# Kernel optimization log

Hardware: AMD Instinct MI355X
Metric: run time of the kernel (lower is better)

Reference implementation:

```python
import jax, jax.numpy as jnp
import numpy as np

B, S, D, H = 2, 2048, 1024, 16
DK = D // H

def setup_inputs() -> dict:
    key = jax.random.key(0)
    ks = jax.random.split(key, 9)
    scale = 1.0 / np.sqrt(D)
    return {
        "x": jax.random.normal(ks[0], (B, S, D), dtype=jnp.float32),
        "Wq": jax.random.uniform(ks[1], (D, D), jnp.float32, -scale, scale),
        "bq": jax.random.uniform(ks[2], (D,), jnp.float32, -scale, scale),
        "Wk": jax.random.uniform(ks[3], (D, D), jnp.float32, -scale, scale),
        "bk": jax.random.uniform(ks[4], (D,), jnp.float32, -scale, scale),
        "Wv": jax.random.uniform(ks[5], (D, D), jnp.float32, -scale, scale),
        "bv": jax.random.uniform(ks[6], (D,), jnp.float32, -scale, scale),
        "Wo": jax.random.uniform(ks[7], (D, D), jnp.float32, -scale, scale),
        "bo": jax.random.uniform(ks[8], (D,), jnp.float32, -scale, scale),
    }

def reference(x, Wq, bq, Wk, bk, Wv, bv, Wo, bo):
    # QKV projections (torch Linear: x @ W.T + b)
    q = x @ Wq.T + bq
    k = x @ Wk.T + bk
    v = x @ Wv.T + bv
    # [B, H, S, DK]
    q = q.reshape(B, S, H, DK).transpose(0, 2, 1, 3)
    k = k.reshape(B, S, H, DK).transpose(0, 2, 1, 3)
    v = v.reshape(B, S, H, DK).transpose(0, 2, 1, 3)
    scores = jnp.einsum('bhqd,bhkd->bhqk', q, k) / jnp.sqrt(jnp.float32(DK))
    p = jax.nn.softmax(scores, axis=-1)  # dropout is identity in eval mode
    o = jnp.einsum('bhqk,bhkd->bhqd', p, v)
    o = o.transpose(0, 2, 1, 3).reshape(B, S, D)
    return o @ Wo.T + bo
```

## Files before the change

### kernel.cpp

```cpp
#include <hip/hip_runtime.h>


typedef __attribute__((ext_vector_type(8))) short short8;
typedef __attribute__((ext_vector_type(4))) float f32x4;
typedef __attribute__((ext_vector_type(8))) unsigned short u16x8;

__device__ __forceinline__ unsigned short f2bf(float f) {
    unsigned int u = __builtin_bit_cast(unsigned int, f);
    u += 0x7FFFu + ((u >> 16) & 1u);
    return (unsigned short)(u >> 16);
}

__device__ __forceinline__ float exp2_fast(float x) {
    return __builtin_amdgcn_exp2f(x);
}

__device__ __forceinline__ void gload16(const void* gsrc, void* ldst) {
    __builtin_amdgcn_global_load_lds(
        (const __attribute__((address_space(1))) unsigned int*)gsrc,
        (__attribute__((address_space(3))) unsigned int*)ldst, 16, 0, 0);
}

__global__ void cast_all(const float* __restrict__ x,
                         const float* __restrict__ wq, const float* __restrict__ wk,
                         const float* __restrict__ wv, const float* __restrict__ wo,
                         unsigned short* __restrict__ xb,
                         unsigned short* __restrict__ wqb, unsigned short* __restrict__ wkb,
                         unsigned short* __restrict__ wvb, unsigned short* __restrict__ wob)
{
    const int z = blockIdx.y;
    const float* src; unsigned short* dst; int n4;
    if (z == 0)      { src = x;  dst = xb;  n4 = 4096 * 1024 / 4; }
    else if (z == 1) { src = wq; dst = wqb; n4 = 1024 * 1024 / 4; }
    else if (z == 2) { src = wk; dst = wkb; n4 = 1024 * 1024 / 4; }
    else if (z == 3) { src = wv; dst = wvb; n4 = 1024 * 1024 / 4; }
    else             { src = wo; dst = wob; n4 = 1024 * 1024 / 4; }
    int i = blockIdx.x * blockDim.x + threadIdx.x;
    if (i < n4) {
        float4 v = reinterpret_cast<const float4*>(src)[i];
        ushort4 o;
        o.x = f2bf(v.x); o.y = f2bf(v.y); o.z = f2bf(v.z); o.w = f2bf(v.w);
        reinterpret_cast<ushort4*>(dst)[i] = o;
    }
}

__global__ __launch_bounds__(256, 2)
void qkv_gemm(const unsigned short* __restrict__ A,
              const unsigned short* __restrict__ Wq_,
              const unsigned short* __restrict__ Wk_,
              const unsigned short* __restrict__ Wv_,
              const float* __restrict__ bq_,
              const float* __restrict__ bk_,
              const float* __restrict__ bv_,
              unsigned short* __restrict__ Qb,
              unsigned short* __restrict__ Kb,
              unsigned short* __restrict__ Vtb)
{
    const int K = 1024;
    __shared__ __align__(16) unsigned short As[128][64];
    __shared__ __align__(16) unsigned short Bs[128][64];

    const int z = blockIdx.z;
    const unsigned short* Bw = (z == 0) ? Wq_ : (z == 1) ? Wk_ : Wv_;
    const float* bias = (z == 0) ? bq_ : (z == 1) ? bk_ : bv_;
    unsigned short* dst = (z == 0) ? Qb : (z == 1) ? Kb : Vtb;
    const float alpha = (z == 0) ? 0.125f * 1.44269504088896340736f : 1.0f;

    const int tid  = threadIdx.x;
    const int lane = tid & 63;
    const int wave = tid >> 6;
    const int wm = (wave >> 1) * 64;
    const int wn = (wave & 1) * 64;
    const int rowBase = blockIdx.y * 128;
    const int colBase = blockIdx.x * 128;
    const int l15 = lane & 15;
    const int lg  = lane >> 4;

    const int srow   = lane >> 3;
    const int schunk = lane & 7;
    const int gchunk = schunk ^ srow;

    f32x4 acc[4][4] = {};

    for (int kt = 0; kt < K; kt += 64) {
        __syncthreads();
#pragma unroll
        for (int it = 0; it < 4; ++it) {
            int r = wave * 8 + it * 32 + srow;
            gload16(A  + (size_t)(rowBase + r) * K + kt + gchunk * 8, &As[wave * 8 + it * 32][0]);
            gload16(Bw + (size_t)(colBase + r) * K + kt + gchunk * 8, &Bs[wave * 8 + it * 32][0]);
        }
        __syncthreads();
#pragma unroll
        for (int kk = 0; kk < 2; ++kk) {
            short8 af[4], bf[4];
#pragma unroll
            for (int fm = 0; fm < 4; ++fm) {
                int r  = wm + fm * 16 + l15;
                int kb = (kk * 4 + lg) ^ (r & 7);
                af[fm] = *reinterpret_cast<const short8*>(&As[r][kb * 8]);
            }
#pragma unroll
            for (int fn = 0; fn < 4; ++fn) {
                int r  = wn + fn * 16 + l15;
                int kb = (kk * 4 + lg) ^ (r & 7);
                bf[fn] = *reinterpret_cast<const short8*>(&Bs[r][kb * 8]);
            }
#pragma unroll
            for (int fm = 0; fm < 4; ++fm)
#pragma unroll
                for (int fn = 0; fn < 4; ++fn)
                    acc[fm][fn] = __builtin_amdgcn_mfma_f32_16x16x32_bf16(
                        af[fm], bf[fn], acc[fm][fn], 0, 0, 0);
        }
    }

#pragma unroll
    for (int fm = 0; fm < 4; ++fm)
#pragma unroll
        for (int fn = 0; fn < 4; ++fn)
#pragma unroll
            for (int r = 0; r < 4; ++r) {
                int grow = rowBase + wm + fm * 16 + lg * 4 + r;
                int gcol = colBase + wn + fn * 16 + l15;
                float v = (acc[fm][fn][r] + bias[gcol]) * alpha;
                int b = grow >> 11, s = grow & 2047;
                int h = gcol >> 6,  dk = gcol & 63;
                if (z < 2)
                    dst[(((size_t)b * 16 + h) * 2048 + s) * 64 + dk] = f2bf(v);
                else
                    dst[(((size_t)b * 16 + h) * 64 + dk) * 2048 + s] = f2bf(v);
            }
}

__global__ __launch_bounds__(256, 2)
void gemm_out(const unsigned short* __restrict__ A,
              const unsigned short* __restrict__ Bw,
              const float* __restrict__ bias,
              float* __restrict__ Cout, int M, int N, int K)
{
    __shared__ __align__(16) unsigned short As[128][64];
    __shared__ __align__(16) unsigned short Bs[128][64];

    const int tid  = threadIdx.x;
    const int lane = tid & 63;
    const int wave = tid >> 6;
    const int wm = (wave >> 1) * 64;
    const int wn = (wave & 1) * 64;
    const int rowBase = blockIdx.y * 128;
    const int colBase = blockIdx.x * 128;
    const int l15 = lane & 15;
    const int lg  = lane >> 4;

    const int srow   = lane >> 3;
    const int schunk = lane & 7;
    const int gchunk = schunk ^ srow;

    f32x4 acc[4][4] = {};

    for (int kt = 0; kt < K; kt += 64) {
        __syncthreads();
#pragma unroll
        for (int it = 0; it < 4; ++it) {
            int r = wave * 8 + it * 32 + srow;
            gload16(A  + (size_t)(rowBase + r) * K + kt + gchunk * 8, &As[wave * 8 + it * 32][0]);
            gload16(Bw + (size_t)(colBase + r) * K + kt + gchunk * 8, &Bs[wave * 8 + it * 32][0]);
        }
        __syncthreads();
#pragma unroll
        for (int kk = 0; kk < 2; ++kk) {
            short8 af[4], bf[4];
#pragma unroll
            for (int fm = 0; fm < 4; ++fm) {
                int r  = wm + fm * 16 + l15;
                int kb = (kk * 4 + lg) ^ (r & 7);
                af[fm] = *reinterpret_cast<const short8*>(&As[r][kb * 8]);
            }
#pragma unroll
            for (int fn = 0; fn < 4; ++fn) {
                int r  = wn + fn * 16 + l15;
                int kb = (kk * 4 + lg) ^ (r & 7);
                bf[fn] = *reinterpret_cast<const short8*>(&Bs[r][kb * 8]);
            }
#pragma unroll
            for (int fm = 0; fm < 4; ++fm)
#pragma unroll
                for (int fn = 0; fn < 4; ++fn)
                    acc[fm][fn] = __builtin_amdgcn_mfma_f32_16x16x32_bf16(
                        af[fm], bf[fn], acc[fm][fn], 0, 0, 0);
        }
    }

#pragma unroll
    for (int fm = 0; fm < 4; ++fm)
#pragma unroll
        for (int fn = 0; fn < 4; ++fn)
#pragma unroll
            for (int r = 0; r < 4; ++r) {
                int grow = rowBase + wm + fm * 16 + lg * 4 + r;
                int gcol = colBase + wn + fn * 16 + l15;
                Cout[(size_t)grow * N + gcol] = acc[fm][fn][r] + bias[gcol];
            }
}

__global__ __launch_bounds__(256, 2)
void attn_kernel(const unsigned short* __restrict__ Q,
                 const unsigned short* __restrict__ Kt,
                 const unsigned short* __restrict__ Vt,
                 unsigned short* __restrict__ O)
{
    __shared__ __align__(16) unsigned short Ks[128][64];
    __shared__ __align__(16) unsigned short Vs[64][128];
    __shared__ __align__(16) unsigned short Ps[4][32][128];

    const int bh = blockIdx.y;
    const int qt = blockIdx.x;
    const int tid  = threadIdx.x;
    const int lane = tid & 63;
    const int w    = tid >> 6;
    const int l15 = lane & 15;
    const int lg  = lane >> 4;

    const unsigned short* Qbh = Q  + (size_t)bh * 2048 * 64;
    const unsigned short* Kbh = Kt + (size_t)bh * 2048 * 64;
    const unsigned short* Vbh = Vt + (size_t)bh * 64 * 2048;

    short8 qf[2][2];
#pragma unroll
    for (int fq = 0; fq < 2; ++fq)
#pragma unroll
        for (int kk = 0; kk < 2; ++kk) {
            int row = qt * 128 + w * 32 + fq * 16 + l15;
            qf[fq][kk] = *reinterpret_cast<const short8*>(
                Qbh + (size_t)row * 64 + kk * 32 + lg * 8);
        }

    float mst[2] = {-1e30f, -1e30f};
    float lst[2] = {0.f, 0.f};
    f32x4 accO[2][4] = {};

    const int sr  = tid >> 3, skb = tid & 7;
    const int vr  = tid >> 4, vkb = tid & 15;

    unsigned short* PsW = &Ps[w][0][0];

    u16x8 kst[4], vst[4];
#pragma unroll
    for (int it = 0; it < 4; ++it)
        kst[it] = *reinterpret_cast<const u16x8*>(Kbh + (size_t)(sr + it * 32) * 64 + skb * 8);
#pragma unroll
    for (int it = 0; it < 4; ++it)
        vst[it] = *reinterpret_cast<const u16x8*>(Vbh + (size_t)(vr + it * 16) * 2048 + vkb * 8);

    for (int t = 0; t < 16; ++t) {
        __syncthreads();
#pragma unroll
        for (int it = 0; it < 4; ++it) {
            int r = sr + it * 32;
            *reinterpret_cast<u16x8*>(&Ks[r][(skb ^ (r & 7)) * 8]) = kst[it];
        }
#pragma unroll
        for (int it = 0; it < 4; ++it) {
            int r = vr + it * 16;
            *reinterpret_cast<u16x8*>(&Vs[r][(vkb ^ (r & 15)) * 8]) = vst[it];
        }
        __syncthreads();

        if (t < 15) {
#pragma unroll
            for (int it = 0; it < 4; ++it)
                kst[it] = *reinterpret_cast<const u16x8*>(
                    Kbh + (size_t)((t + 1) * 128 + sr + it * 32) * 64 + skb * 8);
#pragma unroll
            for (int it = 0; it < 4; ++it)
                vst[it] = *reinterpret_cast<const u16x8*>(
                    Vbh + (size_t)(vr + it * 16) * 2048 + (t + 1) * 128 + vkb * 8);
        }

        f32x4 accS[8][2] = {};
#pragma unroll
        for (int kk = 0; kk < 2; ++kk) {
            short8 kf[8];
#pragma unroll
            for (int fk = 0; fk < 8; ++fk) {
                int r  = fk * 16 + l15;
                int kb = (kk * 4 + lg) ^ (r & 7);
                kf[fk] = *reinterpret_cast<const short8*>(&Ks[r][kb * 8]);
            }
#pragma unroll
            for (int fk = 0; fk < 8; ++fk)
#pragma unroll
                for (int fq = 0; fq < 2; ++fq)
                    accS[fk][fq] = __builtin_amdgcn_mfma_f32_16x16x32_bf16(
                        kf[fk], qf[fq][kk], accS[fk][fq], 0, 0, 0);
        }

        float corrs[2];
#pragma unroll
        for (int fq = 0; fq < 2; ++fq) {
            float mx = -1e30f;
#pragma unroll
            for (int fk = 0; fk < 8; ++fk)
#pragma unroll
                for (int r = 0; r < 4; ++r) mx = fmaxf(mx, accS[fk][fq][r]);
            mx = fmaxf(mx, __shfl_xor(mx, 16));
            mx = fmaxf(mx, __shfl_xor(mx, 32));
            float newm = fmaxf(mst[fq], mx);
            float corr = exp2_fast(mst[fq] - newm);
            mst[fq] = newm; corrs[fq] = corr;
            const int ql = fq * 16 + l15;
            float psum = 0.f;
#pragma unroll
            for (int fk = 0; fk < 8; ++fk)
#pragma unroll
                for (int r = 0; r < 4; ++r) {
                    float p = exp2_fast(accS[fk][fq][r] - newm);
                    psum += p;
                    int k = fk * 16 + lg * 4 + r;
                    PsW[ql * 128 + ((k >> 3) ^ (ql & 7)) * 8 + (k & 7)] = f2bf(p);
                }
            psum += __shfl_xor(psum, 16);
            psum += __shfl_xor(psum, 32);
            lst[fq] = lst[fq] * corr + psum;
        }

        asm volatile("" ::: "memory");

#pragma unroll
        for (int fq = 0; fq < 2; ++fq)
#pragma unroll
            for (int r = 0; r < 4; ++r) {
                float cq = __shfl(corrs[fq], lg * 4 + r);
#pragma unroll
                for (int fd = 0; fd < 4; ++fd) accO[fq][fd][r] *= cq;
            }

#pragma unroll
        for (int kkp = 0; kkp < 4; ++kkp) {
            short8 pf[2], vf[4];
#pragma unroll
            for (int fq = 0; fq < 2; ++fq) {
                int ql = fq * 16 + l15;
                int c  = (kkp * 4 + lg) ^ (ql & 7);
                pf[fq] = *reinterpret_cast<const short8*>(
                    reinterpret_cast<char*>(PsW) + ql * 256 + c * 16);
            }
#pragma unroll
            for (int fd = 0; fd < 4; ++fd) {
                int row = fd * 16 + l15;
                int kb  = (kkp * 4 + lg) ^ (row & 15);
                vf[fd] = *reinterpret_cast<const short8*>(&Vs[row][kb * 8]);
            }
#pragma unroll
            for (int fq = 0; fq < 2; ++fq)
#pragma unroll
                for (int fd = 0; fd < 4; ++fd)
                    accO[fq][fd] = __builtin_amdgcn_mfma_f32_16x16x32_bf16(
                        pf[fq], vf[fd], accO[fq][fd], 0, 0, 0);
        }
    }

    const int b = bh >> 4, h = bh & 15;
#pragma unroll
    for (int fq = 0; fq < 2; ++fq)
#pragma unroll
        for (int r = 0; r < 4; ++r) {
            float linv = 1.0f / __shfl(lst[fq], lg * 4 + r);
            int s = qt * 128 + w * 32 + fq * 16 + lg * 4 + r;
#pragma unroll
            for (int fd = 0; fd < 4; ++fd) {
                int dk = fd * 16 + l15;
                O[((size_t)b * 2048 + s) * 1024 + h * 64 + dk] = f2bf(accO[fq][fd][r] * linv);
            }
        }
}

extern "C" void kernel_launch(void* const* d_in, const int* in_sizes, int n_in,
                              void* d_out, int out_size, void* d_ws, size_t ws_size,
                              hipStream_t stream)
{
    const float* x  = (const float*)d_in[0];
    const float* Wq = (const float*)d_in[1];
    const float* bq = (const float*)d_in[2];
    const float* Wk = (const float*)d_in[3];
    const float* bk = (const float*)d_in[4];
    const float* Wv = (const float*)d_in[5];
    const float* bv = (const float*)d_in[6];
    const float* Wo = (const float*)d_in[7];
    const float* bo = (const float*)d_in[8];
    float* out = (float*)d_out;

    char* ws = (char*)d_ws;
    unsigned short* xb  = (unsigned short*)(ws);
    unsigned short* wqb = (unsigned short*)(ws + ((size_t)8  << 20));
    unsigned short* wkb = (unsigned short*)(ws + ((size_t)10 << 20));
    unsigned short* wvb = (unsigned short*)(ws + ((size_t)12 << 20));
    unsigned short* wob = (unsigned short*)(ws + ((size_t)14 << 20));
    unsigned short* Qb  = (unsigned short*)(ws + ((size_t)16 << 20));
    unsigned short* Kb  = (unsigned short*)(ws + ((size_t)24 << 20));
    unsigned short* Vtb = (unsigned short*)(ws + ((size_t)32 << 20));
    unsigned short* Ob  = (unsigned short*)(ws + ((size_t)40 << 20));

    cast_all<<<dim3(4096, 5), 256, 0, stream>>>(x, Wq, Wk, Wv, Wo,
                                                xb, wqb, wkb, wvb, wob);

    qkv_gemm<<<dim3(8, 32, 3), 256, 0, stream>>>(xb, wqb, wkb, wvb, bq, bk, bv,
                                                 Qb, Kb, Vtb);

    attn_kernel<<<dim3(16, 32), 256, 0, stream>>>(Qb, Kb, Vtb, Ob);

    gemm_out<<<dim3(8, 32), 256, 0, stream>>>(Ob, wob, bo, out, 4096, 1024, 1024);
}
```

Before: 132.9 us.

## Halve attention query tile to 64 rows and split P staging into halves

The attention kernel now processes 16 query rows per wave (64 per block) instead of 32, doubling the grid to 1024 blocks and raising launch bounds to 4 blocks per CU. The P tile buffer shrinks, and the softmax/PV work is split into two 64-key halves with packed 8-byte P stores, reducing register and LDS pressure. The aim is higher occupancy and better latency hiding. In exchange, each K/V tile loaded into LDS is reused by half as many queries, so total K/V global traffic doubles.

```diff
diff --git a/kernel.cpp b/kernel.cpp
--- a/kernel.cpp
+++ b/kernel.cpp
@@ -2,8 +2,10 @@
 
 
 typedef __attribute__((ext_vector_type(8))) short short8;
+typedef __attribute__((ext_vector_type(4))) short short4v;
 typedef __attribute__((ext_vector_type(4))) float f32x4;
 typedef __attribute__((ext_vector_type(8))) unsigned short u16x8;
+typedef __attribute__((ext_vector_type(2))) unsigned int u32x2;
 
 __device__ __forceinline__ unsigned short f2bf(float f) {
     unsigned int u = __builtin_bit_cast(unsigned int, f);
@@ -203,7 +205,7 @@
             }
 }
 
-__global__ __launch_bounds__(256, 2)
+__global__ __launch_bounds__(256, 4)
 void attn_kernel(const unsigned short* __restrict__ Q,
                  const unsigned short* __restrict__ Kt,
                  const unsigned short* __restrict__ Vt,
@@ -211,7 +213,7 @@
 {
     __shared__ __align__(16) unsigned short Ks[128][64];
     __shared__ __align__(16) unsigned short Vs[64][128];
-    __shared__ __align__(16) unsigned short Ps[4][32][128];
+    __shared__ __align__(16) unsigned short Ps[4][16][64];
 
     const int bh = blockIdx.y;
     const int qt = blockIdx.x;
@@ -225,24 +227,23 @@
     const unsigned short* Kbh = Kt + (size_t)bh * 2048 * 64;
     const unsigned short* Vbh = Vt + (size_t)bh * 64 * 2048;
 
-    short8 qf[2][2];
-#pragma unroll
-    for (int fq = 0; fq < 2; ++fq)
-#pragma unroll
-        for (int kk = 0; kk < 2; ++kk) {
-            int row = qt * 128 + w * 32 + fq * 16 + l15;
-            qf[fq][kk] = *reinterpret_cast<const short8*>(
-                Qbh + (size_t)row * 64 + kk * 32 + lg * 8);
-        }
-
-    float mst[2] = {-1e30f, -1e30f};
-    float lst[2] = {0.f, 0.f};
-    f32x4 accO[2][4] = {};
+    short8 qf[2];
+#pragma unroll
+    for (int kk = 0; kk < 2; ++kk) {
+        int row = qt * 64 + w * 16 + l15;
+        qf[kk] = *reinterpret_cast<const short8*>(
+            Qbh + (size_t)row * 64 + kk * 32 + lg * 8);
+    }
+
+    float mst = -1e30f;
+    float lst = 0.f;
+    f32x4 accO[4] = {};
 
     const int sr  = tid >> 3, skb = tid & 7;
     const int vr  = tid >> 4, vkb = tid & 15;
 
     unsigned short* PsW = &Ps[w][0][0];
+    const int ql = l15;
 
     u16x8 kst[4], vst[4];
 #pragma unroll
@@ -277,7 +278,7 @@
                     Vbh + (size_t)(vr + it * 16) * 2048 + (t + 1) * 128 + vkb * 8);
         }
 
-        f32x4 accS[8][2] = {};
+        f32x4 accS[8] = {};
 #pragma unroll
         for (int kk = 0; kk < 2; ++kk) {
             short8 kf[8];
@@ -289,90 +290,85 @@
             }
 #pragma unroll
             for (int fk = 0; fk < 8; ++fk)
-#pragma unroll
-                for (int fq = 0; fq < 2; ++fq)
-                    accS[fk][fq] = __builtin_amdgcn_mfma_f32_16x16x32_bf16(
-                        kf[fk], qf[fq][kk], accS[fk][fq], 0, 0, 0);
-        }
-
-        float corrs[2];
-#pragma unroll
-        for (int fq = 0; fq < 2; ++fq) {
-            float mx = -1e30f;
-#pragma unroll
-            for (int fk = 0; fk < 8; ++fk)
-#pragma unroll
-                for (int r = 0; r < 4; ++r) mx = fmaxf(mx, accS[fk][fq][r]);
-            mx = fmaxf(mx, __shfl_xor(mx, 16));
-            mx = fmaxf(mx, __shfl_xor(mx, 32));
-            float newm = fmaxf(mst[fq], mx);
-            float corr = exp2_fast(mst[fq] - newm);
-            mst[fq] = newm; corrs[fq] = corr;
-            const int ql = fq * 16 + l15;
-            float psum = 0.f;
-#pragma unroll
-            for (int fk = 0; fk < 8; ++fk)
-#pragma unroll
-                for (int r = 0; r < 4; ++r) {
-                    float p = exp2_fast(accS[fk][fq][r] - newm);
-                    psum += p;
-                    int k = fk * 16 + lg * 4 + r;
-                    PsW[ql * 128 + ((k >> 3) ^ (ql & 7)) * 8 + (k & 7)] = f2bf(p);
+                accS[fk] = __builtin_amdgcn_mfma_f32_16x16x32_bf16(
+                    kf[fk], qf[kk], accS[fk], 0, 0, 0);
+        }
+
+        float mx = -1e30f;
+#pragma unroll
+        for (int fk = 0; fk < 8; ++fk)
+#pragma unroll
+            for (int r = 0; r < 4; ++r) mx = fmaxf(mx, accS[fk][r]);
+        mx = fmaxf(mx, __shfl_xor(mx, 16));
+        mx = fmaxf(mx, __shfl_xor(mx, 32));
+        float newm = fmaxf(mst, mx);
+        float corr = exp2_fast(mst - newm);
+        mst = newm;
+
+#pragma unroll
+        for (int r = 0; r < 4; ++r) {
+            float cq = __shfl(corr, lg * 4 + r);
+#pragma unroll
+            for (int fd = 0; fd < 4; ++fd) accO[fd][r] *= cq;
+        }
+
+        float psum = 0.f;
+#pragma unroll
+        for (int hh = 0; hh < 2; ++hh) {
+#pragma unroll
+            for (int f2 = 0; f2 < 4; ++f2) {
+                int fk = hh * 4 + f2;
+                float p0 = exp2_fast(accS[fk][0] - newm);
+                float p1 = exp2_fast(accS[fk][1] - newm);
+                float p2 = exp2_fast(accS[fk][2] - newm);
+                float p3 = exp2_fast(accS[fk][3] - newm);
+                psum += (p0 + p1) + (p2 + p3);
+                unsigned int lo = (unsigned int)f2bf(p0) | ((unsigned int)f2bf(p1) << 16);
+                unsigned int hi = (unsigned int)f2bf(p2) | ((unsigned int)f2bf(p3) << 16);
+                u32x2 tmp; tmp.x = lo; tmp.y = hi;
+                short4v pk = __builtin_bit_cast(short4v, tmp);
+                int c = (f2 * 2 + (lg >> 1)) ^ (ql & 7);
+                *reinterpret_cast<short4v*>(
+                    reinterpret_cast<char*>(PsW) + ql * 128 + c * 16 + (lg & 1) * 8) = pk;
+            }
+            asm volatile("" ::: "memory");
+
+#pragma unroll
+            for (int k2 = 0; k2 < 2; ++k2) {
+                short8 pf, vf[4];
+                int c = (k2 * 4 + lg) ^ (ql & 7);
+                pf = *reinterpret_cast<const short8*>(
+                    reinterpret_cast<char*>(PsW) + ql * 128 + c * 16);
+#pragma unroll
+                for (int fd = 0; fd < 4; ++fd) {
+                    int row = fd * 16 + l15;
+                    int kb  = ((hh * 2 + k2) * 4 + lg) ^ (row & 15);
+                    vf[fd] = *reinterpret_cast<const short8*>(&Vs[row][kb * 8]);
                 }
-            psum += __shfl_xor(psum, 16);
-            psum += __shfl_xor(psum, 32);
-            lst[fq] = lst[fq] * corr + psum;
-        }
-
-        asm volatile("" ::: "memory");
-
-#pragma unroll
-        for (int fq = 0; fq < 2; ++fq)
-#pragma unroll
-            for (int r = 0; r < 4; ++r) {
-                float cq = __shfl(corrs[fq], lg * 4 + r);
-#pragma unroll
-                for (int fd = 0; fd < 4; ++fd) accO[fq][fd][r] *= cq;
-            }
-
-#pragma unroll
-        for (int kkp = 0; kkp < 4; ++kkp) {
-            short8 pf[2], vf[4];
-#pragma unroll
-            for (int fq = 0; fq < 2; ++fq) {
-                int ql = fq * 16 + l15;
-                int c  = (kkp * 4 + lg) ^ (ql & 7);
-                pf[fq] = *reinterpret_cast<const short8*>(
-                    reinterpret_cast<char*>(PsW) + ql * 256 + c * 16);
-            }
-#pragma unroll
-            for (int fd = 0; fd < 4; ++fd) {
-                int row = fd * 16 + l15;
-                int kb  = (kkp * 4 + lg) ^ (row & 15);
-                vf[fd] = *reinterpret_cast<const short8*>(&Vs[row][kb * 8]);
-            }
-#pragma unroll
-            for (int fq = 0; fq < 2; ++fq)
 #pragma unroll
                 for (int fd = 0; fd < 4; ++fd)
-                    accO[fq][fd] = __builtin_amdgcn_mfma_f32_16x16x32_bf16(
-                        pf[fq], vf[fd], accO[fq][fd], 0, 0, 0);
-        }
+                    accO[fd] = __builtin_amdgcn_mfma_f32_16x16x32_bf16(
+                        pf, vf[fd], accO[fd], 0, 0, 0);
+            }
+            asm volatile("" ::: "memory");
+        }
+
+        psum += __shfl_xor(psum, 16);
+        psum += __shfl_xor(psum, 32);
+        lst = lst * corr + psum;
     }
 
     const int b = bh >> 4, h = bh & 15;
 #pragma unroll
-    for (int fq = 0; fq < 2; ++fq)
-#pragma unroll
-        for (int r = 0; r < 4; ++r) {
-            float linv = 1.0f / __shfl(lst[fq], lg * 4 + r);
-            int s = qt * 128 + w * 32 + fq * 16 + lg * 4 + r;
-#pragma unroll
-            for (int fd = 0; fd < 4; ++fd) {
-                int dk = fd * 16 + l15;
-                O[((size_t)b * 2048 + s) * 1024 + h * 64 + dk] = f2bf(accO[fq][fd][r] * linv);
-            }
-        }
+    for (int r = 0; r < 4; ++r) {
+        float linv = 1.0f / __shfl(lst, lg * 4 + r);
+        int s = qt * 64 + w * 16 + lg * 4 + r;
+#pragma unroll
+        for (int fd = 0; fd < 4; ++fd) {
+            int dk = fd * 16 + l15;
+            O[((size_t)b * 2048 + s) * 1024 + h * 64 + dk] = f2bf(accO[fd][r] * linv);
+        }
+    }
 }
 
 extern "C" void kernel_launch(void* const* d_in, const int* in_sizes, int n_in,
@@ -407,7 +403,7 @@
     qkv_gemm<<<dim3(8, 32, 3), 256, 0, stream>>>(xb, wqb, wkb, wvb, bq, bk, bv,
                                                  Qb, Kb, Vtb);
 
-    attn_kernel<<<dim3(16, 32), 256, 0, stream>>>(Qb, Kb, Vtb, Ob);
+    attn_kernel<<<dim3(32, 32), 256, 0, stream>>>(Qb, Kb, Vtb, Ob);
 
     gemm_out<<<dim3(8, 32), 256, 0, stream>>>(Ob, wob, bo, out, 4096, 1024, 1024);
 }
```

New measurement: 180.5 us. 35.8% more time.

## Split P staging into two halves and pack bf16 stores as 64-bit writes

Applied to the files above, without the earlier changes.

The softmax P tile in the attention kernel is now written to LDS and consumed by the PV MFMAs in two 64-key halves, which halves the per-wave P buffer and lets exp computation of one half interleave with MFMAs of the other. P values are packed four at a time into 8-byte stores in place of individual 2-byte stores, and the row-sum reduction is deferred to the end of the tile. Rescaling of the output accumulator moves ahead of the exp work. The extra compiler barriers between halves may limit how much reordering the scheduler can do.

```diff
diff --git a/kernel.cpp b/kernel.cpp
--- a/kernel.cpp
+++ b/kernel.cpp
@@ -2,8 +2,10 @@
 
 
 typedef __attribute__((ext_vector_type(8))) short short8;
+typedef __attribute__((ext_vector_type(4))) short short4v;
 typedef __attribute__((ext_vector_type(4))) float f32x4;
 typedef __attribute__((ext_vector_type(8))) unsigned short u16x8;
+typedef __attribute__((ext_vector_type(2))) unsigned int u32x2;
 
 __device__ __forceinline__ unsigned short f2bf(float f) {
     unsigned int u = __builtin_bit_cast(unsigned int, f);
@@ -211,7 +213,7 @@
 {
     __shared__ __align__(16) unsigned short Ks[128][64];
     __shared__ __align__(16) unsigned short Vs[64][128];
-    __shared__ __align__(16) unsigned short Ps[4][32][128];
+    __shared__ __align__(16) unsigned short Ps[4][32][64];
 
     const int bh = blockIdx.y;
     const int qt = blockIdx.x;
@@ -295,7 +297,7 @@
                         kf[fk], qf[fq][kk], accS[fk][fq], 0, 0, 0);
         }
 
-        float corrs[2];
+        float newms[2], psums[2] = {0.f, 0.f};
 #pragma unroll
         for (int fq = 0; fq < 2; ++fq) {
             float mx = -1e30f;
@@ -307,56 +309,72 @@
             mx = fmaxf(mx, __shfl_xor(mx, 32));
             float newm = fmaxf(mst[fq], mx);
             float corr = exp2_fast(mst[fq] - newm);
-            mst[fq] = newm; corrs[fq] = corr;
-            const int ql = fq * 16 + l15;
-            float psum = 0.f;
-#pragma unroll
-            for (int fk = 0; fk < 8; ++fk)
-#pragma unroll
-                for (int r = 0; r < 4; ++r) {
-                    float p = exp2_fast(accS[fk][fq][r] - newm);
-                    psum += p;
-                    int k = fk * 16 + lg * 4 + r;
-                    PsW[ql * 128 + ((k >> 3) ^ (ql & 7)) * 8 + (k & 7)] = f2bf(p);
+            mst[fq] = newm; newms[fq] = newm;
+            lst[fq] *= corr;
+#pragma unroll
+            for (int r = 0; r < 4; ++r) {
+                float cq = __shfl(corr, lg * 4 + r);
+#pragma unroll
+                for (int fd = 0; fd < 4; ++fd) accO[fq][fd][r] *= cq;
+            }
+        }
+
+#pragma unroll
+        for (int hh = 0; hh < 2; ++hh) {
+#pragma unroll
+            for (int fq = 0; fq < 2; ++fq) {
+                const int ql = fq * 16 + l15;
+#pragma unroll
+                for (int f2 = 0; f2 < 4; ++f2) {
+                    int fk = hh * 4 + f2;
+                    float p0 = exp2_fast(accS[fk][fq][0] - newms[fq]);
+                    float p1 = exp2_fast(accS[fk][fq][1] - newms[fq]);
+                    float p2 = exp2_fast(accS[fk][fq][2] - newms[fq]);
+                    float p3 = exp2_fast(accS[fk][fq][3] - newms[fq]);
+                    psums[fq] += (p0 + p1) + (p2 + p3);
+                    unsigned int lo = (unsigned int)f2bf(p0) | ((unsigned int)f2bf(p1) << 16);
+                    unsigned int hi = (unsigned int)f2bf(p2) | ((unsigned int)f2bf(p3) << 16);
+                    u32x2 tmp; tmp.x = lo; tmp.y = hi;
+                    short4v pk = __builtin_bit_cast(short4v, tmp);
+                    int c = (f2 * 2 + (lg >> 1)) ^ (ql & 7);
+                    *reinterpret_cast<short4v*>(
+                        reinterpret_cast<char*>(PsW) + ql * 128 + c * 16 + (lg & 1) * 8) = pk;
                 }
-            psum += __shfl_xor(psum, 16);
-            psum += __shfl_xor(psum, 32);
-            lst[fq] = lst[fq] * corr + psum;
-        }
-
-        asm volatile("" ::: "memory");
-
-#pragma unroll
-        for (int fq = 0; fq < 2; ++fq)
-#pragma unroll
-            for (int r = 0; r < 4; ++r) {
-                float cq = __shfl(corrs[fq], lg * 4 + r);
-#pragma unroll
-                for (int fd = 0; fd < 4; ++fd) accO[fq][fd][r] *= cq;
-            }
-
-#pragma unroll
-        for (int kkp = 0; kkp < 4; ++kkp) {
-            short8 pf[2], vf[4];
-#pragma unroll
-            for (int fq = 0; fq < 2; ++fq) {
-                int ql = fq * 16 + l15;
-                int c  = (kkp * 4 + lg) ^ (ql & 7);
-                pf[fq] = *reinterpret_cast<const short8*>(
-                    reinterpret_cast<char*>(PsW) + ql * 256 + c * 16);
-            }
-#pragma unroll
-            for (int fd = 0; fd < 4; ++fd) {
-                int row = fd * 16 + l15;
-                int kb  = (kkp * 4 + lg) ^ (row & 15);
-                vf[fd] = *reinterpret_cast<const short8*>(&Vs[row][kb * 8]);
-            }
-#pragma unroll
-            for (int fq = 0; fq < 2; ++fq)
-#pragma unroll
-                for (int fd = 0; fd < 4; ++fd)
-                    accO[fq][fd] = __builtin_amdgcn_mfma_f32_16x16x32_bf16(
-                        pf[fq], vf[fd], accO[fq][fd], 0, 0, 0);
+            }
+            asm volatile("" ::: "memory");
+
+#pragma unroll
+            for (int k2 = 0; k2 < 2; ++k2) {
+                short8 pf[2], vf[4];
+#pragma unroll
+                for (int fq = 0; fq < 2; ++fq) {
+                    int ql = fq * 16 + l15;
+                    int c  = (k2 * 4 + lg) ^ (ql & 7);
+                    pf[fq] = *reinterpret_cast<const short8*>(
+                        reinterpret_cast<char*>(PsW) + ql * 128 + c * 16);
+                }
+#pragma unroll
+                for (int fd = 0; fd < 4; ++fd) {
+                    int row = fd * 16 + l15;
+                    int kb  = ((hh * 2 + k2) * 4 + lg) ^ (row & 15);
+                    vf[fd] = *reinterpret_cast<const short8*>(&Vs[row][kb * 8]);
+                }
+#pragma unroll
+                for (int fq = 0; fq < 2; ++fq)
+#pragma unroll
+                    for (int fd = 0; fd < 4; ++fd)
+                        accO[fq][fd] = __builtin_amdgcn_mfma_f32_16x16x32_bf16(
+                            pf[fq], vf[fd], accO[fq][fd], 0, 0, 0);
+            }
+            asm volatile("" ::: "memory");
+        }
+
+#pragma unroll
+        for (int fq = 0; fq < 2; ++fq) {
+            float ps = psums[fq];
+            ps += __shfl_xor(ps, 16);
+            ps += __shfl_xor(ps, 32);
+            lst[fq] += ps;
         }
     }
 
```

Measured after the change: 131.0 us. No clear change (-1.4%).
